# Kernel optimization log

Hardware: AMD Instinct MI355X
Metric: run time of the kernel (lower is better)

## Reference

```python
import jax, jax.numpy as jnp
import numpy as np

K = 4      # number of per-slot Linear layers (self.k)
H = 512    # hidden_dim
B = 4      # branching factor at every tree level (B >= K -> no padded slots)
T = 1024   # number of trees (roots)
D = 3      # pooled tree levels (= idx_matrix.shape[1] - 2)
N0 = T * B ** D  # 65536 leaves


def _make_level(n_in):
    """Replicates the torch order_matrix / pooling construction for groups of size B.
    order[m, i] = group_base + (pos_in_group + m) % B, then +1 for the zero pad row.
    seg[i] = group id (torch.repeat_interleave of counts)."""
    i = np.arange(n_in)
    base = (i // B) * B
    pos = i % B
    m = np.arange(K)[:, None]
    order = base[None, :] + (pos[None, :] + m) % B + 1  # [K, n_in], all valid since B >= K
    seg = i // B
    return order.astype(np.int32), seg.astype(np.int32)


def setup_inputs() -> dict:
    key = jax.random.key(0)
    ks = jax.random.split(key, 5)
    x = jax.random.normal(ks[0], (N0, H), jnp.float32)
    node_idx = jnp.arange(N0, dtype=jnp.int32)  # idx_matrix[:, -1]
    o1, s1 = _make_level(N0)
    o2, s2 = _make_level(N0 // B)
    o3, s3 = _make_level(N0 // B // B)
    Wz = jax.random.normal(ks[1], (K, H, H), jnp.float32) / np.sqrt(H)   # k slot Linears
    bz = jax.random.normal(ks[2], (K, H), jnp.float32) * 0.02
    Wzf = jax.random.normal(ks[3], (H, H), jnp.float32) / np.sqrt(H)     # z_final_layer
    bzf = jax.random.normal(ks[4], (H,), jnp.float32) * 0.02
    return dict(x=x, Wz=Wz, bz=bz, Wzf=Wzf, bzf=bzf, node_idx=node_idx,
                order1=jnp.asarray(o1), order2=jnp.asarray(o2), order3=jnp.asarray(o3),
                seg1=jnp.asarray(s1), seg2=jnp.asarray(s2), seg3=jnp.asarray(s3))


def _tree_layer(data, order, seg, num_seg, Wz, bz, Wzf, bzf):
    # prepend zero row so padded entries (order == 0) gather zeros
    padded = jnp.concatenate([jnp.zeros((1, data.shape[-1]), data.dtype), data], axis=0)
    emb = padded[order]                                    # [K, N, H] gather
    emb = jnp.einsum('knh,kjh->nkj', emb, Wz) + bz[None]   # per-slot Linear (x @ W.T + b)
    emb = jnp.where((order.T == 0)[..., None], jnp.zeros((), emb.dtype), emb)  # mask padded slots
    emb = emb.sum(axis=1)                                  # sum over K slots -> [N, H]
    emb = emb @ Wzf.T + bzf                                # z_final_layer
    return jax.ops.segment_sum(emb, seg, num_segments=num_seg)  # global_add_pool


def reference(x, Wz, bz, Wzf, bzf, node_idx, order1, order2, order3, seg1, seg2, seg3):
    data = x[node_idx]
    for order, seg in ((order1, seg1), (order2, seg2), (order3, seg3)):
        data = _tree_layer(data, order, seg, order.shape[1] // B, Wz, bz, Wzf, bzf)
    return data  # [T, H]
```

## Files before the change

kernel.cpp:

```cpp
#include <hip/hip_runtime.h>


#define HD 512
#define LDT 68

struct GemmSmem {
    float As[2][32][LDT];
    float Bs[2][32][LDT];
};

template<int MODE>
__device__ __forceinline__
void gemm_tile(const float* __restrict__ A, const float* __restrict__ B,
               float* __restrict__ C, const float* __restrict__ bias,
               float bscale, int i0, int j0, GemmSmem& sm) {
    const int tid  = threadIdx.x;
    const int tx   = tid & 15, ty = tid >> 4;
    const int arow = tid >> 2, akq = (tid & 3) << 2;
    const int bk   = tid >> 4, bc4 = (tid & 15) << 2;

    float4 ap0, ap1, bp0, bp1;

    auto load_tiles = [&](int k0) {
        const float* ar = &A[(size_t)(i0 + arow) * HD + k0 + akq];
        ap0 = *(const float4*)ar;
        ap1 = *(const float4*)(ar + 16);
        if (MODE == 2) {
            const float* br = &B[(size_t)(j0 + arow) * HD + k0 + akq];
            bp0 = *(const float4*)br;
            bp1 = *(const float4*)(br + 16);
        } else if (MODE == 0) {
            bp0 = *(const float4*)&B[(size_t)(k0 + bk) * HD + j0 + bc4];
            bp1 = *(const float4*)&B[(size_t)(k0 + bk + 16) * HD + j0 + bc4];
        } else {
            const float* b0 = &B[(size_t)(k0 + bk) * HD + j0 + bc4];
            const float* b1 = b0 + 16 * HD;
            float4 s0 = *(const float4*)b0, s1 = *(const float4*)b1;
            #pragma unroll
            for (int q = 1; q < 4; ++q) {
                float4 t0 = *(const float4*)(b0 + q * 262144);
                float4 t1 = *(const float4*)(b1 + q * 262144);
                s0.x += t0.x; s0.y += t0.y; s0.z += t0.z; s0.w += t0.w;
                s1.x += t1.x; s1.y += t1.y; s1.z += t1.z; s1.w += t1.w;
            }
            bp0 = s0; bp1 = s1;
        }
    };
    auto store_tiles = [&](int buf) {
        sm.As[buf][akq + 0][arow]  = ap0.x;
        sm.As[buf][akq + 1][arow]  = ap0.y;
        sm.As[buf][akq + 2][arow]  = ap0.z;
        sm.As[buf][akq + 3][arow]  = ap0.w;
        sm.As[buf][akq + 16][arow] = ap1.x;
        sm.As[buf][akq + 17][arow] = ap1.y;
        sm.As[buf][akq + 18][arow] = ap1.z;
        sm.As[buf][akq + 19][arow] = ap1.w;
        if (MODE == 2) {
            sm.Bs[buf][akq + 0][arow]  = bp0.x;
            sm.Bs[buf][akq + 1][arow]  = bp0.y;
            sm.Bs[buf][akq + 2][arow]  = bp0.z;
            sm.Bs[buf][akq + 3][arow]  = bp0.w;
            sm.Bs[buf][akq + 16][arow] = bp1.x;
            sm.Bs[buf][akq + 17][arow] = bp1.y;
            sm.Bs[buf][akq + 18][arow] = bp1.z;
            sm.Bs[buf][akq + 19][arow] = bp1.w;
        } else {
            *(float4*)&sm.Bs[buf][bk][bc4]      = bp0;
            *(float4*)&sm.Bs[buf][bk + 16][bc4] = bp1;
        }
    };

    float acc[4][4] = {};
    load_tiles(0);
    store_tiles(0);
    __syncthreads();

    for (int t = 0; t < 16; ++t) {
        if (t < 15) load_tiles((t + 1) << 5);
        const int cur = t & 1;
        #pragma unroll
        for (int kk = 0; kk < 32; ++kk) {
            float4 av = *(const float4*)&sm.As[cur][kk][ty << 2];
            float4 bv = *(const float4*)&sm.Bs[cur][kk][tx << 2];
            float aa[4] = {av.x, av.y, av.z, av.w};
            float bb[4] = {bv.x, bv.y, bv.z, bv.w};
            #pragma unroll
            for (int i = 0; i < 4; ++i)
                #pragma unroll
                for (int j = 0; j < 4; ++j)
                    acc[i][j] += aa[i] * bb[j];
        }
        if (t < 15) {
            store_tiles(1 - cur);
            __syncthreads();
        }
    }

    float4 bv = make_float4(0.f, 0.f, 0.f, 0.f);
    if (bias) {
        float4 tb = *(const float4*)&bias[j0 + (tx << 2)];
        bv.x = bscale * tb.x; bv.y = bscale * tb.y;
        bv.z = bscale * tb.z; bv.w = bscale * tb.w;
    }
    #pragma unroll
    for (int r = 0; r < 4; ++r) {
        const int row = i0 + (ty << 2) + r;
        float4 o;
        o.x = acc[r][0] + bv.x; o.y = acc[r][1] + bv.y;
        o.z = acc[r][2] + bv.z; o.w = acc[r][3] + bv.w;
        *(float4*)&C[(size_t)row * HD + j0 + (tx << 2)] = o;
    }
}

__device__ __forceinline__
void pool_body(const float* __restrict__ x, float* __restrict__ P3,
               int tree, float4* red) {
    const int tid = threadIdx.x;
    const float4* xp = (const float4*)x + (size_t)tree * 8192 + tid;
    float4 a0 = make_float4(0.f, 0.f, 0.f, 0.f), a1 = a0;
    #pragma unroll
    for (int g = 0; g < 4; ++g) {
        float4 v[8];
        #pragma unroll
        for (int i = 0; i < 8; ++i) v[i] = xp[(size_t)(g * 8 + i) * 256];
        #pragma unroll
        for (int i = 0; i < 8; i += 2) {
            a0.x += v[i].x;     a0.y += v[i].y;
            a0.z += v[i].z;     a0.w += v[i].w;
            a1.x += v[i + 1].x; a1.y += v[i + 1].y;
            a1.z += v[i + 1].z; a1.w += v[i + 1].w;
        }
    }
    a0.x += a1.x; a0.y += a1.y; a0.z += a1.z; a0.w += a1.w;
    if (tid >= 128) red[tid - 128] = a0;
    __syncthreads();
    if (tid < 128) {
        float4 b = red[tid];
        a0.x += b.x; a0.y += b.y; a0.z += b.z; a0.w += b.w;
        ((float4*)P3)[tree * 128 + tid] = a0;
    }
}

__global__ __launch_bounds__(256) void k_stage1(
        const float* __restrict__ x, const float* __restrict__ Wz,
        const float* __restrict__ Wzf, const float* __restrict__ bz,
        const float* __restrict__ bzf,
        float* __restrict__ P3, float* __restrict__ M, float* __restrict__ c0) {
    __shared__ GemmSmem sm;
    const int b = blockIdx.x, tid = threadIdx.x;
    if (b < 64) {
        gemm_tile<1>(Wzf, Wz, M, nullptr, 0.f, (b >> 3) << 6, (b & 7) << 6, sm);
    } else if (b < 1088) {
        pool_body(x, P3, b - 64, (float4*)&sm);
    } else {
        const int j = (b - 1088) * 4 + (tid >> 6);
        const int lane = tid & 63, hb = lane << 3;
        float4 s0 = *(const float4*)&bz[hb];
        float4 s1 = *(const float4*)&bz[hb + 4];
        #pragma unroll
        for (int q = 1; q < 4; ++q) {
            float4 t0 = *(const float4*)&bz[q * HD + hb];
            float4 t1 = *(const float4*)&bz[q * HD + hb + 4];
            s0.x += t0.x; s0.y += t0.y; s0.z += t0.z; s0.w += t0.w;
            s1.x += t1.x; s1.y += t1.y; s1.z += t1.z; s1.w += t1.w;
        }
        const float4* wr = (const float4*)&Wzf[(size_t)j * HD + hb];
        float4 w0 = wr[0], w1 = wr[1];
        float p = w0.x * s0.x + w0.y * s0.y + w0.z * s0.z + w0.w * s0.w
                + w1.x * s1.x + w1.y * s1.y + w1.z * s1.z + w1.w * s1.w;
        #pragma unroll
        for (int off = 32; off > 0; off >>= 1) p += __shfl_down(p, off);
        if (lane == 0) c0[j] = 4.f * (p + bzf[j]);
    }
}

__global__ __launch_bounds__(256) void k_stage2(
        const float* __restrict__ M, const float* __restrict__ P3,
        const float* __restrict__ c0,
        float* __restrict__ M2, float* __restrict__ Y1, float* __restrict__ u) {
    __shared__ GemmSmem sm;
    const int b = blockIdx.x, tid = threadIdx.x;
    if (b < 128) {
        gemm_tile<2>(P3, M, Y1, c0, 16.f, (b >> 3) << 6, (b & 7) << 6, sm);
    } else if (b < 192) {
        const int bb = b - 128;
        gemm_tile<0>(M, M, M2, nullptr, 0.f, (bb >> 3) << 6, (bb & 7) << 6, sm);
    } else {
        const int j = (b - 192) * 4 + (tid >> 6);
        const int lane = tid & 63, hb = lane << 3;
        const float4* mr = (const float4*)&M[(size_t)j * HD + hb];
        const float4* cr = (const float4*)&c0[hb];
        float4 m0 = mr[0], m1 = mr[1], q0 = cr[0], q1 = cr[1];
        float p = m0.x * q0.x + m0.y * q0.y + m0.z * q0.z + m0.w * q0.w
                + m1.x * q1.x + m1.y * q1.y + m1.z * q1.z + m1.w * q1.w;
        #pragma unroll
        for (int off = 32; off > 0; off >>= 1) p += __shfl_down(p, off);
        if (lane == 0) u[j] = 4.f * p + c0[j];
    }
}

__global__ __launch_bounds__(256) void k_stage3(
        const float* __restrict__ Y1, const float* __restrict__ M2,
        const float* __restrict__ u, float* __restrict__ out) {
    __shared__ GemmSmem sm;
    const int b = blockIdx.x;
    gemm_tile<2>(Y1, M2, out, u, 1.f, (b >> 3) << 6, (b & 7) << 6, sm);
}

extern "C" void kernel_launch(void* const* d_in, const int* in_sizes, int n_in,
                              void* d_out, int out_size, void* d_ws, size_t ws_size,
                              hipStream_t stream) {
    const float* x   = (const float*)d_in[0];
    const float* Wz  = (const float*)d_in[1];
    const float* bz  = (const float*)d_in[2];
    const float* Wzf = (const float*)d_in[3];
    const float* bzf = (const float*)d_in[4];
    float* out = (float*)d_out;

    float* ws = (float*)d_ws;
    float* P3 = ws;
    float* Y1 = ws + 524288;
    float* M  = ws + 1048576;
    float* M2 = ws + 1310720;
    float* c0 = ws + 1572864;
    float* u  = ws + 1573376;

    hipLaunchKernelGGL(k_stage1, dim3(1216), dim3(256), 0, stream,
                       x, Wz, Wzf, bz, bzf, P3, M, c0);
    hipLaunchKernelGGL(k_stage2, dim3(320), dim3(256), 0, stream,
                       M, P3, c0, M2, Y1, u);
    hipLaunchKernelGGL(k_stage3, dim3(128), dim3(256), 0, stream,
                       Y1, M2, u, out);
}
```

Before: 296.6 us.

## Halve block size to 128 threads with 8x4 micro-tiles per thread

Measured after the change: 375.4 us. 1.27x slower.

```diff
diff --git a/kernel.cpp b/kernel.cpp
--- a/kernel.cpp
+++ b/kernel.cpp
@@ -15,62 +15,63 @@
                float* __restrict__ C, const float* __restrict__ bias,
                float bscale, int i0, int j0, GemmSmem& sm) {
     const int tid  = threadIdx.x;
-    const int tx   = tid & 15, ty = tid >> 4;
-    const int arow = tid >> 2, akq = (tid & 3) << 2;
-    const int bk   = tid >> 4, bc4 = (tid & 15) << 2;
-
-    float4 ap0, ap1, bp0, bp1;
+    const int cg   = tid & 15, rg = tid >> 4;
+    const int srow = tid >> 1, skq = (tid & 1) << 2;
+    const int bsk  = tid >> 4, bsc4 = (tid & 15) << 2;
+
+    float4 ap[4], bp[4];
 
     auto load_tiles = [&](int k0) {
-        const float* ar = &A[(size_t)(i0 + arow) * HD + k0 + akq];
-        ap0 = *(const float4*)ar;
-        ap1 = *(const float4*)(ar + 16);
+        const float* ar = &A[(size_t)(i0 + srow) * HD + k0 + skq];
+        #pragma unroll
+        for (int p = 0; p < 4; ++p) ap[p] = *(const float4*)(ar + 8 * p);
         if (MODE == 2) {
-            const float* br = &B[(size_t)(j0 + arow) * HD + k0 + akq];
-            bp0 = *(const float4*)br;
-            bp1 = *(const float4*)(br + 16);
+            const float* br = &B[(size_t)(j0 + srow) * HD + k0 + skq];
+            #pragma unroll
+            for (int p = 0; p < 4; ++p) bp[p] = *(const float4*)(br + 8 * p);
         } else if (MODE == 0) {
-            bp0 = *(const float4*)&B[(size_t)(k0 + bk) * HD + j0 + bc4];
-            bp1 = *(const float4*)&B[(size_t)(k0 + bk + 16) * HD + j0 + bc4];
+            const float* br = &B[(size_t)(k0 + bsk) * HD + j0 + bsc4];
+            #pragma unroll
+            for (int p = 0; p < 4; ++p) bp[p] = *(const float4*)(br + 8 * p * HD);
         } else {
-            const float* b0 = &B[(size_t)(k0 + bk) * HD + j0 + bc4];
-            const float* b1 = b0 + 16 * HD;
-            float4 s0 = *(const float4*)b0, s1 = *(const float4*)b1;
-            #pragma unroll
-            for (int q = 1; q < 4; ++q) {
-                float4 t0 = *(const float4*)(b0 + q * 262144);
-                float4 t1 = *(const float4*)(b1 + q * 262144);
-                s0.x += t0.x; s0.y += t0.y; s0.z += t0.z; s0.w += t0.w;
-                s1.x += t1.x; s1.y += t1.y; s1.z += t1.z; s1.w += t1.w;
+            const float* br = &B[(size_t)(k0 + bsk) * HD + j0 + bsc4];
+            #pragma unroll
+            for (int p = 0; p < 4; ++p) {
+                const float* b0 = br + 8 * p * HD;
+                float4 s = *(const float4*)b0;
+                #pragma unroll
+                for (int q = 1; q < 4; ++q) {
+                    float4 t = *(const float4*)(b0 + q * 262144);
+                    s.x += t.x; s.y += t.y; s.z += t.z; s.w += t.w;
+                }
+                bp[p] = s;
             }
-            bp0 = s0; bp1 = s1;
         }
     };
     auto store_tiles = [&](int buf) {
-        sm.As[buf][akq + 0][arow]  = ap0.x;
-        sm.As[buf][akq + 1][arow]  = ap0.y;
-        sm.As[buf][akq + 2][arow]  = ap0.z;
-        sm.As[buf][akq + 3][arow]  = ap0.w;
-        sm.As[buf][akq + 16][arow] = ap1.x;
-        sm.As[buf][akq + 17][arow] = ap1.y;
-        sm.As[buf][akq + 18][arow] = ap1.z;
-        sm.As[buf][akq + 19][arow] = ap1.w;
+        #pragma unroll
+        for (int p = 0; p < 4; ++p) {
+            sm.As[buf][skq + 8 * p + 0][srow] = ap[p].x;
+            sm.As[buf][skq + 8 * p + 1][srow] = ap[p].y;
+            sm.As[buf][skq + 8 * p + 2][srow] = ap[p].z;
+            sm.As[buf][skq + 8 * p + 3][srow] = ap[p].w;
+        }
         if (MODE == 2) {
-            sm.Bs[buf][akq + 0][arow]  = bp0.x;
-            sm.Bs[buf][akq + 1][arow]  = bp0.y;
-            sm.Bs[buf][akq + 2][arow]  = bp0.z;
-            sm.Bs[buf][akq + 3][arow]  = bp0.w;
-            sm.Bs[buf][akq + 16][arow] = bp1.x;
-            sm.Bs[buf][akq + 17][arow] = bp1.y;
-            sm.Bs[buf][akq + 18][arow] = bp1.z;
-            sm.Bs[buf][akq + 19][arow] = bp1.w;
+            #pragma unroll
+            for (int p = 0; p < 4; ++p) {
+                sm.Bs[buf][skq + 8 * p + 0][srow] = bp[p].x;
+                sm.Bs[buf][skq + 8 * p + 1][srow] = bp[p].y;
+                sm.Bs[buf][skq + 8 * p + 2][srow] = bp[p].z;
+                sm.Bs[buf][skq + 8 * p + 3][srow] = bp[p].w;
+            }
         } else {
-            *(float4*)&sm.Bs[buf][bk][bc4]      = bp0;
-            *(float4*)&sm.Bs[buf][bk + 16][bc4] = bp1;
+            #pragma unroll
+            for (int p = 0; p < 4; ++p)
+                *(float4*)&sm.Bs[buf][bsk + 8 * p][bsc4] = bp[p];
         }
     };
 
-    float acc[4][4] = {};
+    float acc[8][4] = {};
     load_tiles(0);
     store_tiles(0);
     __syncthreads();
@@ -80,12 +81,13 @@
         const int cur = t & 1;
         #pragma unroll
         for (int kk = 0; kk < 32; ++kk) {
-            float4 av = *(const float4*)&sm.As[cur][kk][ty << 2];
-            float4 bv = *(const float4*)&sm.Bs[cur][kk][tx << 2];
-            float aa[4] = {av.x, av.y, av.z, av.w};
+            float4 a0 = *(const float4*)&sm.As[cur][kk][rg << 3];
+            float4 a1 = *(const float4*)&sm.As[cur][kk][(rg << 3) + 4];
+            float4 bv = *(const float4*)&sm.Bs[cur][kk][cg << 2];
+            float aa[8] = {a0.x, a0.y, a0.z, a0.w, a1.x, a1.y, a1.z, a1.w};
             float bb[4] = {bv.x, bv.y, bv.z, bv.w};
             #pragma unroll
-            for (int i = 0; i < 4; ++i)
+            for (int i = 0; i < 8; ++i)
                 #pragma unroll
                 for (int j = 0; j < 4; ++j)
                     acc[i][j] += aa[i] * bb[j];
@@ -98,31 +100,30 @@
 
     float4 bv = make_float4(0.f, 0.f, 0.f, 0.f);
     if (bias) {
-        float4 tb = *(const float4*)&bias[j0 + (tx << 2)];
+        float4 tb = *(const float4*)&bias[j0 + (cg << 2)];
         bv.x = bscale * tb.x; bv.y = bscale * tb.y;
         bv.z = bscale * tb.z; bv.w = bscale * tb.w;
     }
     #pragma unroll
-    for (int r = 0; r < 4; ++r) {
-        const int row = i0 + (ty << 2) + r;
+    for (int r = 0; r < 8; ++r) {
+        const int row = i0 + (rg << 3) + r;
         float4 o;
         o.x = acc[r][0] + bv.x; o.y = acc[r][1] + bv.y;
         o.z = acc[r][2] + bv.z; o.w = acc[r][3] + bv.w;
-        *(float4*)&C[(size_t)row * HD + j0 + (tx << 2)] = o;
-    }
-}
-
-__device__ __forceinline__
-void pool_body(const float* __restrict__ x, float* __restrict__ P3,
-               int tree, float4* red) {
+        *(float4*)&C[(size_t)row * HD + j0 + (cg << 2)] = o;
+    }
+}
+
+__device__ __forceinline__
+void pool_body(const float* __restrict__ x, float* __restrict__ P3, int tree) {
     const int tid = threadIdx.x;
     const float4* xp = (const float4*)x + (size_t)tree * 8192 + tid;
     float4 a0 = make_float4(0.f, 0.f, 0.f, 0.f), a1 = a0;
     #pragma unroll
-    for (int g = 0; g < 4; ++g) {
+    for (int g = 0; g < 8; ++g) {
         float4 v[8];
         #pragma unroll
-        for (int i = 0; i < 8; ++i) v[i] = xp[(size_t)(g * 8 + i) * 256];
+        for (int i = 0; i < 8; ++i) v[i] = xp[(size_t)(g * 8 + i) * 128];
         #pragma unroll
         for (int i = 0; i < 8; i += 2) {
             a0.x += v[i].x;     a0.y += v[i].y;
@@ -132,74 +133,80 @@
         }
     }
     a0.x += a1.x; a0.y += a1.y; a0.z += a1.z; a0.w += a1.w;
-    if (tid >= 128) red[tid - 128] = a0;
-    __syncthreads();
-    if (tid < 128) {
-        float4 b = red[tid];
-        a0.x += b.x; a0.y += b.y; a0.z += b.z; a0.w += b.w;
-        ((float4*)P3)[tree * 128 + tid] = a0;
-    }
-}
-
-__global__ __launch_bounds__(256) void k_stage1(
+    ((float4*)P3)[tree * 128 + tid] = a0;
+}
+
+__device__ __forceinline__
+void c0_body(const float* __restrict__ bz, const float* __restrict__ Wzf,
+             const float* __restrict__ bzf, float* __restrict__ c0, int bb) {
+    const int tid = threadIdx.x, lane = tid & 63, hb = lane << 3;
+    const int j = bb * 2 + (tid >> 6);
+    float4 s0 = *(const float4*)&bz[hb];
+    float4 s1 = *(const float4*)&bz[hb + 4];
+    #pragma unroll
+    for (int q = 1; q < 4; ++q) {
+        float4 t0 = *(const float4*)&bz[q * HD + hb];
+        float4 t1 = *(const float4*)&bz[q * HD + hb + 4];
+        s0.x += t0.x; s0.y += t0.y; s0.z += t0.z; s0.w += t0.w;
+        s1.x += t1.x; s1.y += t1.y; s1.z += t1.z; s1.w += t1.w;
+    }
+    const float4* wr = (const float4*)&Wzf[(size_t)j * HD + hb];
+    float4 w0 = wr[0], w1 = wr[1];
+    float p = w0.x * s0.x + w0.y * s0.y + w0.z * s0.z + w0.w * s0.w
+            + w1.x * s1.x + w1.y * s1.y + w1.z * s1.z + w1.w * s1.w;
+    #pragma unroll
+    for (int off = 32; off > 0; off >>= 1) p += __shfl_down(p, off);
+    if (lane == 0) c0[j] = 4.f * (p + bzf[j]);
+}
+
+__device__ __forceinline__
+void u_body(const float* __restrict__ M, const float* __restrict__ c0,
+            float* __restrict__ u, int bb) {
+    const int tid = threadIdx.x, lane = tid & 63, hb = lane << 3;
+    const int j = bb * 2 + (tid >> 6);
+    const float4* mr = (const float4*)&M[(size_t)j * HD + hb];
+    const float4* cr = (const float4*)&c0[hb];
+    float4 m0 = mr[0], m1 = mr[1], q0 = cr[0], q1 = cr[1];
+    float p = m0.x * q0.x + m0.y * q0.y + m0.z * q0.z + m0.w * q0.w
+            + m1.x * q1.x + m1.y * q1.y + m1.z * q1.z + m1.w * q1.w;
+    #pragma unroll
+    for (int off = 32; off > 0; off >>= 1) p += __shfl_down(p, off);
+    if (lane == 0) u[j] = 4.f * p + c0[j];
+}
+
+__global__ __launch_bounds__(128) void kD1(
         const float* __restrict__ x, const float* __restrict__ Wz,
-        const float* __restrict__ Wzf, const float* __restrict__ bz,
+        const float* __restrict__ bz, const float* __restrict__ Wzf,
         const float* __restrict__ bzf,
         float* __restrict__ P3, float* __restrict__ M, float* __restrict__ c0) {
     __shared__ GemmSmem sm;
-    const int b = blockIdx.x, tid = threadIdx.x;
+    const int b = blockIdx.x;
     if (b < 64) {
         gemm_tile<1>(Wzf, Wz, M, nullptr, 0.f, (b >> 3) << 6, (b & 7) << 6, sm);
     } else if (b < 1088) {
-        pool_body(x, P3, b - 64, (float4*)&sm);
+        pool_body(x, P3, b - 64);
     } else {
-        const int j = (b - 1088) * 4 + (tid >> 6);
-        const int lane = tid & 63, hb = lane << 3;
-        float4 s0 = *(const float4*)&bz[hb];
-        float4 s1 = *(const float4*)&bz[hb + 4];
-        #pragma unroll
-        for (int q = 1; q < 4; ++q) {
-            float4 t0 = *(const float4*)&bz[q * HD + hb];
-            float4 t1 = *(const float4*)&bz[q * HD + hb + 4];
-            s0.x += t0.x; s0.y += t0.y; s0.z += t0.z; s0.w += t0.w;
-            s1.x += t1.x; s1.y += t1.y; s1.z += t1.z; s1.w += t1.w;
-        }
-        const float4* wr = (const float4*)&Wzf[(size_t)j * HD + hb];
-        float4 w0 = wr[0], w1 = wr[1];
-        float p = w0.x * s0.x + w0.y * s0.y + w0.z * s0.z + w0.w * s0.w
-                + w1.x * s1.x + w1.y * s1.y + w1.z * s1.z + w1.w * s1.w;
-        #pragma unroll
-        for (int off = 32; off > 0; off >>= 1) p += __shfl_down(p, off);
-        if (lane == 0) c0[j] = 4.f * (p + bzf[j]);
-    }
-}
-
-__global__ __launch_bounds__(256) void k_stage2(
+        c0_body(bz, Wzf, bzf, c0, b - 1088);
+    }
+}
+
+__global__ __launch_bounds__(128) void kD2(
         const float* __restrict__ M, const float* __restrict__ P3,
         const float* __restrict__ c0,
         float* __restrict__ M2, float* __restrict__ Y1, float* __restrict__ u) {
     __shared__ GemmSmem sm;
-    const int b = blockIdx.x, tid = threadIdx.x;
+    const int b = blockIdx.x;
     if (b < 128) {
         gemm_tile<2>(P3, M, Y1, c0, 16.f, (b >> 3) << 6, (b & 7) << 6, sm);
     } else if (b < 192) {
         const int bb = b - 128;
         gemm_tile<0>(M, M, M2, nullptr, 0.f, (bb >> 3) << 6, (bb & 7) << 6, sm);
     } else {
-        const int j = (b - 192) * 4 + (tid >> 6);
-        const int lane = tid & 63, hb = lane << 3;
-        const float4* mr = (const float4*)&M[(size_t)j * HD + hb];
-        const float4* cr = (const float4*)&c0[hb];
-        float4 m0 = mr[0], m1 = mr[1], q0 = cr[0], q1 = cr[1];
-        float p = m0.x * q0.x + m0.y * q0.y + m0.z * q0.z + m0.w * q0.w
-                + m1.x * q1.x + m1.y * q1.y + m1.z * q1.z + m1.w * q1.w;
-        #pragma unroll
-        for (int off = 32; off > 0; off >>= 1) p += __shfl_down(p, off);
-        if (lane == 0) u[j] = 4.f * p + c0[j];
-    }
-}
-
-__global__ __launch_bounds__(256) void k_stage3(
+        u_body(M, c0, u, b - 192);
+    }
+}
+
+__global__ __launch_bounds__(128) void kD3(
         const float* __restrict__ Y1, const float* __restrict__ M2,
         const float* __restrict__ u, float* __restrict__ out) {
     __shared__ GemmSmem sm;
@@ -225,10 +232,10 @@
     float* c0 = ws + 1572864;
     float* u  = ws + 1573376;
 
-    hipLaunchKernelGGL(k_stage1, dim3(1216), dim3(256), 0, stream,
-                       x, Wz, Wzf, bz, bzf, P3, M, c0);
-    hipLaunchKernelGGL(k_stage2, dim3(320), dim3(256), 0, stream,
+    hipLaunchKernelGGL(kD1, dim3(1344), dim3(128), 0, stream,
+                       x, Wz, bz, Wzf, bzf, P3, M, c0);
+    hipLaunchKernelGGL(kD2, dim3(448), dim3(128), 0, stream,
                        M, P3, c0, M2, Y1, u);
-    hipLaunchKernelGGL(k_stage3, dim3(128), dim3(256), 0, stream,
+    hipLaunchKernelGGL(kD3, dim3(128), dim3(128), 0, stream,
                        Y1, M2, u, out);
 }
```
